# Kernel tuning notes

Measured on AMD Instinct MI355X. Metric: run time of the kernel, lower is better.

## Reference

```python
import jax, jax.numpy as jnp
import numpy as np

N = 100_000   # nodes
E = 1_600_000 # edges
F = 128       # input features
H = 128       # hidden
C = 10        # classes
G = 64        # graphs in batch
NUM_LAYERS = 3


def setup_inputs() -> dict:
    key = jax.random.key(0)
    ks = jax.random.split(key, 16)
    x = jax.random.normal(ks[0], (N, F), jnp.float32)
    edge_index = jax.random.randint(ks[1], (2, E), 0, N, dtype=jnp.int64)
    batch = jnp.sort(jax.random.randint(ks[2], (N,), 0, G, dtype=jnp.int64))
    sF = 1.0 / np.sqrt(F)
    sH = 1.0 / np.sqrt(H)
    return {
        "x": x,
        "edge_index": edge_index,
        "batch": batch,
        # conv1 (main) and convs_random_1 branches
        "W1": jax.random.normal(ks[3], (F, H), jnp.float32) * sF,
        "b1": jnp.zeros((H,), jnp.float32),
        "Wr1": jax.random.normal(ks[4], (F, H), jnp.float32) * sF,
        "br1": jnp.zeros((H,), jnp.float32),
        # num_layers-1 hidden GCNConv layers (distinct weights per layer)
        "W2": jax.random.normal(ks[5], (NUM_LAYERS - 1, H, H), jnp.float32) * sH,
        "b2": jnp.zeros((NUM_LAYERS - 1, H), jnp.float32),
        # single shared random-branch conv for all hidden layers
        "Wr": jax.random.normal(ks[6], (H, H), jnp.float32) * sH,
        "br": jnp.zeros((H,), jnp.float32),
        # readout MLP
        "Wl1": jax.random.normal(ks[7], (H, H), jnp.float32) * sH,
        "bl1": jnp.zeros((H,), jnp.float32),
        "Wl2": jax.random.normal(ks[8], (H, C), jnp.float32) * sH,
        "bl2": jnp.zeros((C,), jnp.float32),
    }


def reference(x, edge_index, batch, W1, b1, Wr1, br1, W2, b2, Wr, br,
              Wl1, bl1, Wl2, bl2):
    src, dst = edge_index[0], edge_index[1]
    # GCN symmetric norm with self-loops: deg = in-degree + 1
    deg = jax.ops.segment_sum(jnp.ones((E,), x.dtype), dst, num_segments=N) + 1.0
    dinv_sqrt = deg ** -0.5
    enorm = (dinv_sqrt[src] * dinv_sqrt[dst])[:, None]   # [E,1]
    self_norm = (1.0 / deg)[:, None]                      # [N,1] self-loop coeff

    def gcn_conv(h, W, b):
        h = h @ W                                         # [N,H]
        agg = jax.ops.segment_sum(h[src] * enorm, dst, num_segments=N)
        return agg + h * self_norm + b

    h = jax.nn.relu(0.95 * gcn_conv(x, W1, b1) + 0.05 * gcn_conv(x, Wr1, br1))
    for i in range(NUM_LAYERS - 1):
        h = jax.nn.relu(0.95 * gcn_conv(h, W2[i], b2[i])
                        + 0.05 * gcn_conv(h, Wr, br))

    # global mean pool over graphs
    counts = jax.ops.segment_sum(jnp.ones((N,), x.dtype), batch, num_segments=G)
    pooled = jax.ops.segment_sum(h, batch, num_segments=G) / jnp.maximum(counts, 1.0)[:, None]

    out = jax.nn.relu(pooled @ Wl1 + bl1)
    # dropout p=0.5 is identity in eval mode
    logits = out @ Wl2 + bl2
    return jax.nn.log_softmax(logits, axis=-1)
```

## Files before the change

kernel.cpp:

```cpp
#include <hip/hip_runtime.h>
#include <hip/hip_bf16.h>
#include <hip/hip_fp8.h>

#define NN 100000
#define NE 1600000
#define FF 128
#define HH 128
#define CC 10
#define GG 64

#define NCHUNK 2048
#define CE 782
#define NBUCKET 128
#define BSPAN 782
#define PSEG 16
#define SRCBITS 17

typedef __attribute__((ext_vector_type(8))) short short8;
typedef __attribute__((ext_vector_type(4))) float f32x4;
typedef __attribute__((ext_vector_type(2))) float f32x2;

__device__ inline unsigned short f2bf(float f) {
    union { float f; unsigned int i; } x;
    x.f = f;
    unsigned int r = x.i + 0x7FFF + ((x.i >> 16) & 1);
    return (unsigned short)(r >> 16);
}
__device__ inline unsigned char f8enc_sw(float v) {
    __hip_fp8_e4m3 q(v);
    return (unsigned char)q.__x;
}
__device__ inline float f8dec(unsigned char b) {
    __hip_fp8_e4m3 q;
    q.__x = (__hip_fp8_storage_t)b;
    return (float)q;
}

#if defined(__has_builtin)
#if __has_builtin(__builtin_amdgcn_cvt_pk_f32_fp8)
#define HAVE_CVT_PK_F32_FP8 1
#endif
#if __has_builtin(__builtin_amdgcn_cvt_pk_fp8_f32)
#define HAVE_CVT_PK_FP8 1
#endif
#endif

__device__ inline void dec8(uint2 v, float* o) {
#ifdef HAVE_CVT_PK_F32_FP8
    f32x2 p;
    p = __builtin_amdgcn_cvt_pk_f32_fp8(v.x, false); o[0] = p[0]; o[1] = p[1];
    p = __builtin_amdgcn_cvt_pk_f32_fp8(v.x, true);  o[2] = p[0]; o[3] = p[1];
    p = __builtin_amdgcn_cvt_pk_f32_fp8(v.y, false); o[4] = p[0]; o[5] = p[1];
    p = __builtin_amdgcn_cvt_pk_f32_fp8(v.y, true);  o[6] = p[0]; o[7] = p[1];
#else
#pragma unroll
    for (int j = 0; j < 4; ++j) {
        o[j]     = f8dec((v.x >> (8 * j)) & 0xFF);
        o[j + 4] = f8dec((v.y >> (8 * j)) & 0xFF);
    }
#endif
}
__device__ inline void dec8p(uint2 v, f32x2* o) {
#ifdef HAVE_CVT_PK_F32_FP8
    o[0] = __builtin_amdgcn_cvt_pk_f32_fp8(v.x, false);
    o[1] = __builtin_amdgcn_cvt_pk_f32_fp8(v.x, true);
    o[2] = __builtin_amdgcn_cvt_pk_f32_fp8(v.y, false);
    o[3] = __builtin_amdgcn_cvt_pk_f32_fp8(v.y, true);
#else
    float d[8]; dec8(v, d);
#pragma unroll
    for (int j = 0; j < 4; ++j) { o[j][0] = d[2 * j]; o[j][1] = d[2 * j + 1]; }
#endif
}
__device__ inline unsigned enc_pk4(float a, float b, float c, float d) {
#ifdef HAVE_CVT_PK_FP8
    int w = __builtin_amdgcn_cvt_pk_fp8_f32(a, b, 0, false);
    w = __builtin_amdgcn_cvt_pk_fp8_f32(c, d, w, true);
    return (unsigned)w;
#else
    return (unsigned)f8enc_sw(a) | ((unsigned)f8enc_sw(b) << 8) |
           ((unsigned)f8enc_sw(c) << 16) | ((unsigned)f8enc_sw(d) << 24);
#endif
}
__device__ inline unsigned char f8enc1(float v) {
#ifdef HAVE_CVT_PK_FP8
    return (unsigned char)(__builtin_amdgcn_cvt_pk_fp8_f32(v, v, 0, false) & 0xFF);
#else
    return f8enc_sw(v);
#endif
}

__global__ __launch_bounds__(256) void combw_kernel(const float* __restrict__ W1, const float* __restrict__ b1,
                                                    const float* __restrict__ Wr1, const float* __restrict__ br1,
                                                    const float* __restrict__ W2, const float* __restrict__ b2,
                                                    const float* __restrict__ Wr, const float* __restrict__ br,
                                                    unsigned short* __restrict__ Wpack, float* __restrict__ bc) {
    int idx = blockIdx.x * 256 + threadIdx.x;
    if (idx >= 3 * 16384) return;
    int l = idx / 16384, rem = idx % 16384;
    int cb = rem / 2048;
    int kb = (rem / 512) % 4;
    int lane = (rem / 8) % 64;
    int j = rem % 8;
    int k = kb * 32 + (lane >> 4) * 8 + j;
    int c = cb * 16 + (lane & 15);
    int wi = k * HH + c;
    float v = (l == 0) ? 0.95f * W1[wi] + 0.05f * Wr1[wi]
                       : 0.95f * W2[(l - 1) * 16384 + wi] + 0.05f * Wr[wi];
    Wpack[idx] = f2bf(v);
    if (rem < HH) {
        bc[l * HH + rem] = (l == 0) ? 0.95f * b1[rem] + 0.05f * br1[rem]
                                    : 0.95f * b2[(l - 1) * HH + rem] + 0.05f * br[rem];
    }
}

__global__ __launch_bounds__(256) void partA1_kernel(const int* __restrict__ ei,
                                                     int* __restrict__ cc) {
    __shared__ int h[NBUCKET];
    int c = blockIdx.x, t = threadIdx.x;
    if (t < NBUCKET) h[t] = 0;
    __syncthreads();
    int beg = c * CE, end = min(beg + CE, NE);
    for (int e = beg + t; e < end; e += 256)
        atomicAdd(&h[ei[NE + e] / BSPAN], 1);
    __syncthreads();
    if (t < NBUCKET) cc[c * NBUCKET + t] = h[t];
}

__global__ __launch_bounds__(256) void partA2_kernel(int* __restrict__ cc,
                                                     int* __restrict__ tot) {
    __shared__ int sh[256];
    int b = blockIdx.x, t = threadIdx.x;
    int v[8]; int s = 0;
#pragma unroll
    for (int i = 0; i < 8; ++i) { v[i] = cc[(t * 8 + i) * NBUCKET + b]; s += v[i]; }
    sh[t] = s; __syncthreads();
    for (int off = 1; off < 256; off <<= 1) {
        int x = (t >= off) ? sh[t - off] : 0; __syncthreads();
        sh[t] += x; __syncthreads();
    }
    int excl = sh[t] - s;
#pragma unroll
    for (int i = 0; i < 8; ++i) {
        cc[(t * 8 + i) * NBUCKET + b] = excl;
        excl += v[i];
    }
    if (t == 255) tot[b] = sh[255];
}

__global__ __launch_bounds__(256) void partA3_kernel(const int* __restrict__ ei,
                                                     const int* __restrict__ cc,
                                                     const int* __restrict__ tot,
                                                     unsigned* __restrict__ eb32) {
    __shared__ int stot[NBUCKET];
    __shared__ int cur[NBUCKET];
    int c = blockIdx.x, t = threadIdx.x;
    if (t < NBUCKET) stot[t] = tot[t];
    __syncthreads();
    for (int off = 1; off < NBUCKET; off <<= 1) {
        int x = (t < NBUCKET && t >= off) ? stot[t - off] : 0;
        __syncthreads();
        if (t < NBUCKET) stot[t] += x;
        __syncthreads();
    }
    if (t < NBUCKET) cur[t] = (stot[t] - tot[t]) + cc[c * NBUCKET + t];
    __syncthreads();
    int beg = c * CE, end = min(beg + CE, NE);
    for (int e = beg + t; e < end; e += 256) {
        int d = ei[NE + e];
        int s = ei[e];
        int b = d / BSPAN;
        int ld = d - b * BSPAN;
        int p = atomicAdd(&cur[b], 1);
        eb32[p] = (unsigned)s | ((unsigned)ld << SRCBITS);
    }
}

__global__ __launch_bounds__(256) void partB_kernel(const unsigned* __restrict__ eb32,
                                                    const int* __restrict__ tot,
                                                    int* __restrict__ offs,
                                                    float* __restrict__ dinv,
                                                    int* __restrict__ csrc) {
    __shared__ int hcnt[BSPAN];
    __shared__ int lcur[BSPAN];
    __shared__ int sh[256];
    __shared__ int gbase_sh;
    int b = blockIdx.x, t = threadIdx.x;
    int lo = b * BSPAN;
    int span = min(BSPAN, NN - lo);
    if (span <= 0) return;
    for (int i = t; i < span; i += 256) hcnt[i] = 0;
    if (t == 0) {
        int g = 0;
        for (int i = 0; i < b; ++i) g += tot[i];
        gbase_sh = g;
    }
    __syncthreads();
    int gbase = gbase_sh;
    int len = tot[b];
    const unsigned* ebb = eb32 + (size_t)gbase;
    for (int e = t; e < len; e += 256)
        atomicAdd(&hcnt[ebb[e] >> SRCBITS], 1);
    __syncthreads();
    int base = t * 4;
    int v[4]; int s = 0;
#pragma unroll
    for (int j = 0; j < 4; ++j) { int i = base + j; v[j] = (i < span) ? hcnt[i] : 0; s += v[j]; }
    sh[t] = s; __syncthreads();
    for (int off = 1; off < 256; off <<= 1) {
        int x = (t >= off) ? sh[t - off] : 0; __syncthreads();
        sh[t] += x; __syncthreads();
    }
    int excl = sh[t] - s + gbase;
#pragma unroll
    for (int j = 0; j < 4; ++j) {
        int i = base + j;
        if (i < span) {
            offs[lo + i] = excl;
            lcur[i] = excl;
            dinv[lo + i] = rsqrtf((float)v[j] + 1.0f);
            excl += v[j];
        }
    }
    if (b == NBUCKET - 1 && t == 0) offs[NN] = NE;
    __syncthreads();
    for (int e = t; e < len; e += 256) {
        unsigned pr = ebb[e];
        int p = atomicAdd(&lcur[pr >> SRCBITS], 1);
        csrc[p] = (int)(pr & ((1u << SRCBITS) - 1));
    }
}

__global__ __launch_bounds__(256) void gemm_f32_kernel(const float* __restrict__ A,
                                                       const unsigned short* __restrict__ Wp,
                                                       const float* __restrict__ dinv,
                                                       unsigned char* __restrict__ out8,
                                                       int nrows) {
    __shared__ unsigned char f8s[64][128];
    int w = threadIdx.x >> 6;
    int l = threadIdx.x & 63;
    int m0 = blockIdx.x * 64 + w * 16;
    int kg = l >> 4;
    int cl = l & 15;
    int arow = m0 + cl;

    short8 a[4];
    if (arow < nrows) {
        const float4* Ar4 = (const float4*)(A + (size_t)arow * HH);
#pragma unroll
        for (int kb = 0; kb < 4; ++kb) {
            float4 u0 = Ar4[kb * 8 + kg * 2];
            float4 u1 = Ar4[kb * 8 + kg * 2 + 1];
            short8 tt;
            tt[0] = (short)f2bf(u0.x); tt[1] = (short)f2bf(u0.y);
            tt[2] = (short)f2bf(u0.z); tt[3] = (short)f2bf(u0.w);
            tt[4] = (short)f2bf(u1.x); tt[5] = (short)f2bf(u1.y);
            tt[6] = (short)f2bf(u1.z); tt[7] = (short)f2bf(u1.w);
            a[kb] = tt;
        }
    } else {
        short8 z = {};
#pragma unroll
        for (int kb = 0; kb < 4; ++kb) a[kb] = z;
    }

    float dv[4];
#pragma unroll
    for (int r = 0; r < 4; ++r) {
        int orow = m0 + kg * 4 + r;
        dv[r] = (orow < nrows) ? dinv[orow] : 0.f;
    }

#pragma unroll
    for (int cb = 0; cb < 8; ++cb) {
        f32x4 acc = {0.f, 0.f, 0.f, 0.f};
#pragma unroll
        for (int kb = 0; kb < 4; ++kb) {
            short8 b = *(const short8*)(Wp + (size_t)(cb * 4 + kb) * 512 + l * 8);
            acc = __builtin_amdgcn_mfma_f32_16x16x32_bf16(a[kb], b, acc, 0, 0, 0);
        }
#pragma unroll
        for (int r = 0; r < 4; ++r)
            f8s[w * 16 + kg * 4 + r][cb * 16 + cl] = f8enc1(acc[r] * dv[r]);
    }
    __syncthreads();
    int blk0 = blockIdx.x * 64;
    for (int u = threadIdx.x; u < 512; u += 256) {
        int row = u >> 3, c16 = u & 7;
        int grow = blk0 + row;
        if (grow < nrows)
            ((uint4*)out8)[(size_t)grow * 8 + c16] = ((const uint4*)&f8s[row][0])[c16];
    }
}

__global__ __launch_bounds__(256) void gemm_mfma_kernel(const unsigned char* __restrict__ A8,
                                                        const unsigned short* __restrict__ Wp,
                                                        const float* __restrict__ dinv,
                                                        unsigned char* __restrict__ out8,
                                                        int nrows) {
    __shared__ unsigned char f8s[64][128];
    int w = threadIdx.x >> 6;
    int l = threadIdx.x & 63;
    int m0 = blockIdx.x * 64 + w * 16;
    int kg = l >> 4;
    int cl = l & 15;
    int arow = m0 + cl;

    short8 a[4];
    if (arow < nrows) {
        const uint2* Ar = (const uint2*)(A8 + (size_t)arow * HH);
#pragma unroll
        for (int kb = 0; kb < 4; ++kb) {
            uint2 v = Ar[kb * 4 + kg];
            float d[8]; dec8(v, d);
            short8 t;
#pragma unroll
            for (int j = 0; j < 8; ++j) t[j] = (short)f2bf(d[j]);
            a[kb] = t;
        }
    } else {
        short8 z = {};
#pragma unroll
        for (int kb = 0; kb < 4; ++kb) a[kb] = z;
    }

    float dv[4];
#pragma unroll
    for (int r = 0; r < 4; ++r) {
        int orow = m0 + kg * 4 + r;
        dv[r] = (orow < nrows) ? dinv[orow] : 0.f;
    }

#pragma unroll
    for (int cb = 0; cb < 8; ++cb) {
        f32x4 acc = {0.f, 0.f, 0.f, 0.f};
#pragma unroll
        for (int kb = 0; kb < 4; ++kb) {
            short8 b = *(const short8*)(Wp + (size_t)(cb * 4 + kb) * 512 + l * 8);
            acc = __builtin_amdgcn_mfma_f32_16x16x32_bf16(a[kb], b, acc, 0, 0, 0);
        }
#pragma unroll
        for (int r = 0; r < 4; ++r)
            f8s[w * 16 + kg * 4 + r][cb * 16 + cl] = f8enc1(acc[r] * dv[r]);
    }
    __syncthreads();
    int blk0 = blockIdx.x * 64;
    for (int u = threadIdx.x; u < 512; u += 256) {
        int row = u >> 3, c16 = u & 7;
        int grow = blk0 + row;
        if (grow < nrows)
            ((uint4*)out8)[(size_t)grow * 8 + c16] = ((const uint4*)&f8s[row][0])[c16];
    }
}

__global__ __launch_bounds__(256) void agg_relu_kernel(const unsigned char* __restrict__ t8,
                                                       const int* __restrict__ offs,
                                                       const int* __restrict__ csrc,
                                                       const float* __restrict__ dinv,
                                                       const float* __restrict__ bias,
                                                       unsigned char* __restrict__ hOut) {
    int n = blockIdx.x * 32 + (threadIdx.x >> 3);
    if (n >= NN) return;
    int lane = threadIdx.x & 7;
    int beg = offs[n], end = offs[n + 1];
    const uint4* g16 = (const uint4*)t8;
    f32x2 acc2[8] = {};
    f32x2 d2[4];
    int e = beg;
    for (; e + 7 < end; e += 8) {
        uint4 v[8];
#pragma unroll
        for (int q = 0; q < 8; ++q)
            v[q] = g16[(size_t)csrc[e + q] * 8 + lane];
#pragma unroll
        for (int q = 0; q < 8; ++q) {
            uint2 a, b;
            a.x = v[q].x; a.y = v[q].y; b.x = v[q].z; b.y = v[q].w;
            dec8p(a, d2);
#pragma unroll
            for (int k = 0; k < 4; ++k) acc2[k] += d2[k];
            dec8p(b, d2);
#pragma unroll
            for (int k = 0; k < 4; ++k) acc2[k + 4] += d2[k];
        }
    }
    for (; e <= end; ++e) {
        int s = (e < end) ? csrc[e] : n;
        uint4 v = g16[(size_t)s * 8 + lane];
        uint2 a, b;
        a.x = v.x; a.y = v.y; b.x = v.z; b.y = v.w;
        dec8p(a, d2);
#pragma unroll
        for (int k = 0; k < 4; ++k) acc2[k] += d2[k];
        dec8p(b, d2);
#pragma unroll
        for (int k = 0; k < 4; ++k) acc2[k + 4] += d2[k];
    }
    float dn = dinv[n];
    const float4* bv = (const float4*)(bias + lane * 16);
    float bb[16];
    float4 b0 = bv[0], b1 = bv[1], b2 = bv[2], b3 = bv[3];
    bb[0]=b0.x; bb[1]=b0.y; bb[2]=b0.z; bb[3]=b0.w;
    bb[4]=b1.x; bb[5]=b1.y; bb[6]=b1.z; bb[7]=b1.w;
    bb[8]=b2.x; bb[9]=b2.y; bb[10]=b2.z; bb[11]=b2.w;
    bb[12]=b3.x; bb[13]=b3.y; bb[14]=b3.z; bb[15]=b3.w;
    float o[16];
#pragma unroll
    for (int j = 0; j < 16; ++j)
        o[j] = fmaxf(fmaf(acc2[j >> 1][j & 1], dn, bb[j]), 0.f);
    uint4 w;
    w.x = enc_pk4(o[0], o[1], o[2], o[3]);
    w.y = enc_pk4(o[4], o[5], o[6], o[7]);
    w.z = enc_pk4(o[8], o[9], o[10], o[11]);
    w.w = enc_pk4(o[12], o[13], o[14], o[15]);
    ((uint4*)hOut)[(size_t)n * 8 + lane] = w;
}

__global__ __launch_bounds__(256) void poolseg_kernel(const unsigned char* __restrict__ h8,
                                                      const int* __restrict__ batch,
                                                      float* __restrict__ psum_seg) {
    int g = blockIdx.x >> 4;
    int seg = blockIdx.x & (PSEG - 1);
    int t = threadIdx.x;
    int lo = 0, hi = NN;
    while (lo < hi) { int m = (lo + hi) >> 1; if (batch[m] < g) lo = m + 1; else hi = m; }
    int lb = lo;
    lo = 0; hi = NN;
    while (lo < hi) { int m = (lo + hi) >> 1; if (batch[m] <= g) lo = m + 1; else hi = m; }
    int ub = lo;
    int len = ub - lb;
    int b0 = lb + (int)(((long long)len * seg) / PSEG);
    int b1 = lb + (int)(((long long)len * (seg + 1)) / PSEG);

    int fg = t & 15;
    int rg = t >> 4;
    const uint2* gp = (const uint2*)h8;
    f32x2 acc2[4] = {};
    f32x2 d2[4];
    for (int n = b0 + rg; n < b1; n += 16) {
        uint2 v = gp[(size_t)n * 16 + fg];
        dec8p(v, d2);
#pragma unroll
        for (int k = 0; k < 4; ++k) acc2[k] += d2[k];
    }
    __shared__ float red[256][8];
#pragma unroll
    for (int j = 0; j < 8; ++j) red[t][j] = acc2[j >> 1][j & 1];
    __syncthreads();
    for (int off = 8; off >= 1; off >>= 1) {
        if (rg < off) {
#pragma unroll
            for (int j = 0; j < 8; ++j) red[t][j] += red[t + off * 16][j];
        }
        __syncthreads();
    }
    if (t < 16) {
#pragma unroll
        for (int j = 0; j < 8; ++j)
            psum_seg[((size_t)g * PSEG + seg) * HH + t * 8 + j] = red[t][j];
    }
}

__global__ __launch_bounds__(128) void mlp2_kernel(const float* __restrict__ psum_seg,
                                                   const int* __restrict__ batch,
                                                   const float* __restrict__ Wl1,
                                                   const float* __restrict__ bl1,
                                                   const float* __restrict__ Wl2,
                                                   const float* __restrict__ bl2,
                                                   float* __restrict__ out) {
    __shared__ float p[128], o1[128], lg[CC];
    int g = blockIdx.x, t = threadIdx.x;
    int lo = 0, hi = NN;
    while (lo < hi) { int m = (lo + hi) >> 1; if (batch[m] < g) lo = m + 1; else hi = m; }
    int lb = lo;
    lo = 0; hi = NN;
    while (lo < hi) { int m = (lo + hi) >> 1; if (batch[m] <= g) lo = m + 1; else hi = m; }
    int len = lo - lb;
    float a = 0.f;
#pragma unroll
    for (int s = 0; s < PSEG; ++s)
        a += psum_seg[((size_t)g * PSEG + s) * HH + t];
    p[t] = a / fmaxf((float)len, 1.f);
    __syncthreads();
    float acc = bl1[t];
    for (int k = 0; k < HH; ++k) acc = fmaf(p[k], Wl1[k * HH + t], acc);
    o1[t] = fmaxf(acc, 0.f);
    __syncthreads();
    if (t < CC) {
        float a2 = bl2[t];
        for (int j = 0; j < HH; ++j) a2 = fmaf(o1[j], Wl2[j * CC + t], a2);
        lg[t] = a2;
    }
    __syncthreads();
    if (t == 0) {
        float m = lg[0];
        for (int c = 1; c < CC; ++c) m = fmaxf(m, lg[c]);
        float s = 0.f;
        for (int c = 0; c < CC; ++c) s += expf(lg[c] - m);
        float ls = logf(s);
        for (int c = 0; c < CC; ++c) out[g * CC + c] = lg[c] - m - ls;
    }
}

extern "C" void kernel_launch(void* const* d_in, const int* in_sizes, int n_in,
                              void* d_out, int out_size, void* d_ws, size_t ws_size,
                              hipStream_t stream) {
    const float* x   = (const float*)d_in[0];
    const int*   ei  = (const int*)d_in[1];
    const int*   bat = (const int*)d_in[2];
    const float* W1  = (const float*)d_in[3];
    const float* b1  = (const float*)d_in[4];
    const float* Wr1 = (const float*)d_in[5];
    const float* br1 = (const float*)d_in[6];
    const float* W2  = (const float*)d_in[7];
    const float* b2  = (const float*)d_in[8];
    const float* Wr  = (const float*)d_in[9];
    const float* br  = (const float*)d_in[10];
    const float* Wl1 = (const float*)d_in[11];
    const float* bl1 = (const float*)d_in[12];
    const float* Wl2 = (const float*)d_in[13];
    const float* bl2 = (const float*)d_in[14];
    float* out = (float*)d_out;

    char* base = (char*)d_ws;
    size_t off = 0;
    auto alloc = [&](size_t bytes) {
        void* p = base + off;
        off += (bytes + 255) & ~(size_t)255;
        return p;
    };
    unsigned char* h8   = (unsigned char*)alloc((size_t)NN * HH);
    unsigned char* t8   = (unsigned char*)alloc((size_t)NN * HH);
    unsigned* eb32 = (unsigned*)alloc((size_t)NE * 4);
    int*   cc     = (int*)alloc((size_t)NCHUNK * NBUCKET * 4);
    int*   csrc   = (int*)alloc((size_t)NE * 4);
    int*   offs   = (int*)alloc((size_t)(NN + 1) * 4);
    float* dinv   = (float*)alloc((size_t)NN * 4);
    int*   tot    = (int*)alloc(NBUCKET * 4);
    unsigned short* Wpack = (unsigned short*)alloc(3 * 16384 * 2);
    float* bc     = (float*)alloc(3 * HH * 4);
    float* psum_seg = (float*)alloc((size_t)GG * PSEG * HH * 4);
    (void)ws_size; (void)in_sizes; (void)n_in; (void)out_size;

    combw_kernel<<<192, 256, 0, stream>>>(W1, b1, Wr1, br1, W2, b2, Wr, br, Wpack, bc);

    partA1_kernel<<<NCHUNK, 256, 0, stream>>>(ei, cc);
    partA2_kernel<<<NBUCKET, 256, 0, stream>>>(cc, tot);
    partA3_kernel<<<NCHUNK, 256, 0, stream>>>(ei, cc, tot, eb32);
    partB_kernel<<<NBUCKET, 256, 0, stream>>>(eb32, tot, offs, dinv, csrc);

    const int GEMM_BLOCKS = (NN + 63) / 64;
    const int AGG_BLOCKS = (NN + 31) / 32;
    gemm_f32_kernel<<<GEMM_BLOCKS, 256, 0, stream>>>(x, Wpack, dinv, t8, NN);
    agg_relu_kernel<<<AGG_BLOCKS, 256, 0, stream>>>(t8, offs, csrc, dinv, bc, h8);
    gemm_mfma_kernel<<<GEMM_BLOCKS, 256, 0, stream>>>(h8, Wpack + 16384, dinv, t8, NN);
    agg_relu_kernel<<<AGG_BLOCKS, 256, 0, stream>>>(t8, offs, csrc, dinv, bc + HH, h8);
    gemm_mfma_kernel<<<GEMM_BLOCKS, 256, 0, stream>>>(h8, Wpack + 2 * 16384, dinv, t8, NN);
    agg_relu_kernel<<<AGG_BLOCKS, 256, 0, stream>>>(t8, offs, csrc, dinv, bc + 2 * HH, h8);

    poolseg_kernel<<<GG * PSEG, 256, 0, stream>>>(h8, bat, psum_seg);
    mlp2_kernel<<<GG, 128, 0, stream>>>(psum_seg, bat, Wl1, bl1, Wl2, bl2, out);
}
```

Measured before the change: 242.7 us.

## Fuse aggregation+ReLU with next layer's MFMA GEMM in one kernel

Merges the per-node aggregation, bias and ReLU of layers 1 and 2 with the following layer's bf16 MFMA transform. The activated rows stay in swizzled LDS as bf16 and never go through a global fp8 round trip. This removes two kernel launches and the h8 write/read between aggregation and GEMM, and it ping-pongs between two t8 buffers. Intermediate activations now feed the GEMM in bf16 rather than fp8, which slightly changes numerics. Each block now does only 32 rows of GEMM, so W fragment reloads per row go up.

```diff
diff --git a/kernel.cpp b/kernel.cpp
--- a/kernel.cpp
+++ b/kernel.cpp
@@ -88,6 +88,9 @@
 #else
     return f8enc_sw(v);
 #endif
+}
+__device__ inline unsigned pack2bf(float a, float b) {
+    return (unsigned)f2bf(a) | ((unsigned)f2bf(b) << 16);
 }
 
 __global__ __launch_bounds__(256) void combw_kernel(const float* __restrict__ W1, const float* __restrict__ b1,
@@ -293,46 +296,101 @@
     }
 }
 
-__global__ __launch_bounds__(256) void gemm_mfma_kernel(const unsigned char* __restrict__ A8,
-                                                        const unsigned short* __restrict__ Wp,
-                                                        const float* __restrict__ dinv,
-                                                        unsigned char* __restrict__ out8,
-                                                        int nrows) {
-    __shared__ unsigned char f8s[64][128];
-    int w = threadIdx.x >> 6;
+__global__ __launch_bounds__(256) void agg_gemm_kernel(const unsigned char* __restrict__ t8in,
+                                                       const int* __restrict__ offs,
+                                                       const int* __restrict__ csrc,
+                                                       const float* __restrict__ dinv,
+                                                       const float* __restrict__ bias,
+                                                       const unsigned short* __restrict__ Wp,
+                                                       unsigned char* __restrict__ t8out) {
+    __shared__ unsigned char hbuf[32 * 256];
+    __shared__ unsigned char f8s[32][128];
+    __shared__ float sdinv[32];
+    int n0 = blockIdx.x * 32;
+    int ln = threadIdx.x >> 3;
+    int lane = threadIdx.x & 7;
+    int n = n0 + ln;
+
+    int beg = offs[n], end = offs[n + 1];
+    const uint4* g16 = (const uint4*)t8in;
+    f32x2 acc2[8] = {};
+    f32x2 d2[4];
+    int e = beg;
+    for (; e + 7 < end; e += 8) {
+        uint4 v[8];
+#pragma unroll
+        for (int q = 0; q < 8; ++q)
+            v[q] = g16[(size_t)csrc[e + q] * 8 + lane];
+#pragma unroll
+        for (int q = 0; q < 8; ++q) {
+            uint2 a, b;
+            a.x = v[q].x; a.y = v[q].y; b.x = v[q].z; b.y = v[q].w;
+            dec8p(a, d2);
+#pragma unroll
+            for (int k = 0; k < 4; ++k) acc2[k] += d2[k];
+            dec8p(b, d2);
+#pragma unroll
+            for (int k = 0; k < 4; ++k) acc2[k + 4] += d2[k];
+        }
+    }
+    for (; e <= end; ++e) {
+        int s = (e < end) ? csrc[e] : n;
+        uint4 v = g16[(size_t)s * 8 + lane];
+        uint2 a, b;
+        a.x = v.x; a.y = v.y; b.x = v.z; b.y = v.w;
+        dec8p(a, d2);
+#pragma unroll
+        for (int k = 0; k < 4; ++k) acc2[k] += d2[k];
+        dec8p(b, d2);
+#pragma unroll
+        for (int k = 0; k < 4; ++k) acc2[k + 4] += d2[k];
+    }
+    float dn = dinv[n];
+    if (lane == 0) sdinv[ln] = dn;
+    const float4* bv = (const float4*)(bias + lane * 16);
+    float bb[16];
+    {
+        float4 b0 = bv[0], b1 = bv[1], b2 = bv[2], b3 = bv[3];
+        bb[0]=b0.x; bb[1]=b0.y; bb[2]=b0.z; bb[3]=b0.w;
+        bb[4]=b1.x; bb[5]=b1.y; bb[6]=b1.z; bb[7]=b1.w;
+        bb[8]=b2.x; bb[9]=b2.y; bb[10]=b2.z; bb[11]=b2.w;
+        bb[12]=b3.x; bb[13]=b3.y; bb[14]=b3.z; bb[15]=b3.w;
+    }
+    float o[16];
+#pragma unroll
+    for (int j = 0; j < 16; ++j)
+        o[j] = fmaxf(fmaf(acc2[j >> 1][j & 1], dn, bb[j]), 0.f);
+    uint4 u0, u1;
+    u0.x = pack2bf(o[0], o[1]);  u0.y = pack2bf(o[2], o[3]);
+    u0.z = pack2bf(o[4], o[5]);  u0.w = pack2bf(o[6], o[7]);
+    u1.x = pack2bf(o[8], o[9]);  u1.y = pack2bf(o[10], o[11]);
+    u1.z = pack2bf(o[12], o[13]); u1.w = pack2bf(o[14], o[15]);
+    unsigned swz = (unsigned)((ln & 7) << 4);
+    unsigned base = (unsigned)ln * 256 + (unsigned)lane * 32;
+    *(uint4*)(hbuf + ((base) ^ swz)) = u0;
+    *(uint4*)(hbuf + ((base + 16) ^ swz)) = u1;
+    __syncthreads();
+
+    int wv = threadIdx.x >> 6;
     int l = threadIdx.x & 63;
-    int m0 = blockIdx.x * 64 + w * 16;
+    int rt = wv & 1;
+    int ch = wv >> 1;
     int kg = l >> 4;
     int cl = l & 15;
-    int arow = m0 + cl;
-
+    int arow = rt * 16 + cl;
+    unsigned rswz = (unsigned)((arow & 7) << 4);
     short8 a[4];
-    if (arow < nrows) {
-        const uint2* Ar = (const uint2*)(A8 + (size_t)arow * HH);
-#pragma unroll
-        for (int kb = 0; kb < 4; ++kb) {
-            uint2 v = Ar[kb * 4 + kg];
-            float d[8]; dec8(v, d);
-            short8 t;
-#pragma unroll
-            for (int j = 0; j < 8; ++j) t[j] = (short)f2bf(d[j]);
-            a[kb] = t;
-        }
-    } else {
-        short8 z = {};
-#pragma unroll
-        for (int kb = 0; kb < 4; ++kb) a[kb] = z;
-    }
-
+#pragma unroll
+    for (int kb = 0; kb < 4; ++kb) {
+        unsigned boff = (unsigned)arow * 256 + (unsigned)kb * 64 + (unsigned)kg * 16;
+        a[kb] = *(const short8*)(hbuf + (boff ^ rswz));
+    }
     float dv[4];
 #pragma unroll
-    for (int r = 0; r < 4; ++r) {
-        int orow = m0 + kg * 4 + r;
-        dv[r] = (orow < nrows) ? dinv[orow] : 0.f;
-    }
-
-#pragma unroll
-    for (int cb = 0; cb < 8; ++cb) {
+    for (int r = 0; r < 4; ++r) dv[r] = sdinv[rt * 16 + kg * 4 + r];
+#pragma unroll
+    for (int q = 0; q < 4; ++q) {
+        int cb = ch * 4 + q;
         f32x4 acc = {0.f, 0.f, 0.f, 0.f};
 #pragma unroll
         for (int kb = 0; kb < 4; ++kb) {
@@ -341,16 +399,11 @@
         }
 #pragma unroll
         for (int r = 0; r < 4; ++r)
-            f8s[w * 16 + kg * 4 + r][cb * 16 + cl] = f8enc1(acc[r] * dv[r]);
-    }
-    __syncthreads();
-    int blk0 = blockIdx.x * 64;
-    for (int u = threadIdx.x; u < 512; u += 256) {
-        int row = u >> 3, c16 = u & 7;
-        int grow = blk0 + row;
-        if (grow < nrows)
-            ((uint4*)out8)[(size_t)grow * 8 + c16] = ((const uint4*)&f8s[row][0])[c16];
-    }
+            f8s[rt * 16 + kg * 4 + r][cb * 16 + cl] = f8enc1(acc[r] * dv[r]);
+    }
+    __syncthreads();
+    int row2 = threadIdx.x >> 3, c16 = threadIdx.x & 7;
+    ((uint4*)t8out)[(size_t)(n0 + row2) * 8 + c16] = ((const uint4*)&f8s[row2][0])[c16];
 }
 
 __global__ __launch_bounds__(256) void agg_relu_kernel(const unsigned char* __restrict__ t8,
@@ -529,8 +582,9 @@
         off += (bytes + 255) & ~(size_t)255;
         return p;
     };
+    unsigned char* t8a  = (unsigned char*)alloc((size_t)NN * HH);
+    unsigned char* t8b  = (unsigned char*)alloc((size_t)NN * HH);
     unsigned char* h8   = (unsigned char*)alloc((size_t)NN * HH);
-    unsigned char* t8   = (unsigned char*)alloc((size_t)NN * HH);
     unsigned* eb32 = (unsigned*)alloc((size_t)NE * 4);
     int*   cc     = (int*)alloc((size_t)NCHUNK * NBUCKET * 4);
     int*   csrc   = (int*)alloc((size_t)NE * 4);
@@ -550,13 +604,13 @@
     partB_kernel<<<NBUCKET, 256, 0, stream>>>(eb32, tot, offs, dinv, csrc);
 
     const int GEMM_BLOCKS = (NN + 63) / 64;
-    const int AGG_BLOCKS = (NN + 31) / 32;
-    gemm_f32_kernel<<<GEMM_BLOCKS, 256, 0, stream>>>(x, Wpack, dinv, t8, NN);
-    agg_relu_kernel<<<AGG_BLOCKS, 256, 0, stream>>>(t8, offs, csrc, dinv, bc, h8);
-    gemm_mfma_kernel<<<GEMM_BLOCKS, 256, 0, stream>>>(h8, Wpack + 16384, dinv, t8, NN);
-    agg_relu_kernel<<<AGG_BLOCKS, 256, 0, stream>>>(t8, offs, csrc, dinv, bc + HH, h8);
-    gemm_mfma_kernel<<<GEMM_BLOCKS, 256, 0, stream>>>(h8, Wpack + 2 * 16384, dinv, t8, NN);
-    agg_relu_kernel<<<AGG_BLOCKS, 256, 0, stream>>>(t8, offs, csrc, dinv, bc + 2 * HH, h8);
+    const int FUSE_BLOCKS = NN / 32;
+    gemm_f32_kernel<<<GEMM_BLOCKS, 256, 0, stream>>>(x, Wpack, dinv, t8a, NN);
+    agg_gemm_kernel<<<FUSE_BLOCKS, 256, 0, stream>>>(t8a, offs, csrc, dinv, bc,
+                                                     Wpack + 16384, t8b);
+    agg_gemm_kernel<<<FUSE_BLOCKS, 256, 0, stream>>>(t8b, offs, csrc, dinv, bc + HH,
+                                                     Wpack + 2 * 16384, t8a);
+    agg_relu_kernel<<<FUSE_BLOCKS, 256, 0, stream>>>(t8a, offs, csrc, dinv, bc + 2 * HH, h8);
 
     poolseg_kernel<<<GG * PSEG, 256, 0, stream>>>(h8, bat, psum_seg);
     mlp2_kernel<<<GG, 128, 0, stream>>>(psum_seg, bat, Wl1, bl1, Wl2, bl2, out);
```

After: 226.2 us. 1.07x faster.
